# Performance work log

Hardware: AMD Instinct MI355X
Metric: run time of the kernel (lower is better)

Reference implementation:

```python
import jax, jax.numpy as jnp
import numpy as np

N, IN_DIM, HID, OUT, E = 20000, 1024, 512, 128, 160000


def _xavier(key, fan_out, fan_in):
    a = (6.0 / (fan_in + fan_out)) ** 0.5
    return jax.random.uniform(key, (fan_out, fan_in), jnp.float32, -a, a)


def setup_inputs() -> dict:
    key = jax.random.key(0)
    ks = jax.random.split(key, 8)
    features = jax.random.normal(ks[0], (N, IN_DIM), jnp.float32)
    edge_index = jax.random.randint(ks[1], (2, E), 0, N, jnp.int64)
    W1 = _xavier(ks[2], HID, IN_DIM)   # conv1.lin.weight [out,in]
    b1 = jnp.zeros((HID,), jnp.float32)
    W2 = _xavier(ks[3], OUT, HID)      # conv2.lin.weight
    b2 = jnp.zeros((OUT,), jnp.float32)
    b3 = jnp.zeros((HID,), jnp.float32)  # conv3 bias (weight tied = W2.T)
    b4 = jnp.zeros((IN_DIM,), jnp.float32)  # conv4 bias (weight tied = W1.T)
    head1 = _xavier(ks[4], OUT, OUT)
    return dict(features=features, edge_index=edge_index, W1=W1, b1=b1,
                W2=W2, b2=b2, b3=b3, b4=b4, head1=head1)


def _gcn_conv(x, W, b, src, dst, norm, n):
    # GCNConv: transform then symmetric-normalized neighbor aggregation
    h = x @ W.T                       # [N, out]
    msg = h[src] * norm[:, None]      # [E', out] gathered + scaled
    out = jax.ops.segment_sum(msg, dst, num_segments=n)
    return out + b


def reference(features, edge_index, W1, b1, W2, b2, b3, b4, head1):
    n = features.shape[0]
    loops = jnp.arange(n, dtype=edge_index.dtype)
    src = jnp.concatenate([edge_index[0], loops])  # add self-loops
    dst = jnp.concatenate([edge_index[1], loops])
    deg = jax.ops.segment_sum(jnp.ones_like(dst, dtype=features.dtype), dst,
                              num_segments=n)
    dinv = jnp.where(deg > 0, deg ** -0.5, 0.0)
    norm = dinv[src] * dinv[dst]

    h1 = _gcn_conv(features, W1, b1, src, dst, norm, n)
    h2 = _gcn_conv(h1, W2, b2, src, dst, norm, n)
    z = h2 @ head1
    # tied weights: conv3.W = W2^T, conv4.W = W1^T
    h3 = _gcn_conv(z, W2.T, b3, src, dst, norm, n)
    h4 = _gcn_conv(h3, W1.T, b4, src, dst, norm, n)
    return z, h2, h4
```

## Files before the change

kernel.cpp:

```cpp
#include <hip/hip_runtime.h>

typedef short   short8  __attribute__((ext_vector_type(8)));
typedef unsigned short ushort8 __attribute__((ext_vector_type(8)));
typedef float   floatx4 __attribute__((ext_vector_type(4)));

__device__ __forceinline__ float bf2f(unsigned short h) {
    unsigned int u = ((unsigned int)h) << 16;
    return __builtin_bit_cast(float, u);
}
__device__ __forceinline__ unsigned short f2bf(float f) {
    unsigned int u = __builtin_bit_cast(unsigned int, f);
    u += 0x7fffu + ((u >> 16) & 1u);
    return (unsigned short)(u >> 16);
}


__global__ __launch_bounds__(256) void k_detect_f32(const unsigned short* __restrict__ X,
                                                    int nPairs, int* __restrict__ flags) {
    int i = blockIdx.x * 256 + threadIdx.x;
    if (i < nPairs) {
        unsigned short w = X[2 * i];
        if ((w & 0x7F80u) == 0x7F80u) atomicOr(&flags[0], 1);
    }
}

__global__ __launch_bounds__(256) void k_detect_i32(const int* __restrict__ ei,
                                                    int E, int* __restrict__ flags) {
    int i = blockIdx.x * 256 + threadIdx.x;
    if (i < E) {
        if (ei[2 * i + 1] != 0) atomicOr(&flags[1], 1);
    }
}


__global__ __launch_bounds__(256) void k_cvt_f32(const void* __restrict__ in,
                                                 float* __restrict__ out, int n,
                                                 const int* __restrict__ flags) {
    int i = blockIdx.x * 256 + threadIdx.x;
    if (i < n)
        out[i] = flags[0] ? ((const float*)in)[i] : bf2f(((const unsigned short*)in)[i]);
}

__global__ __launch_bounds__(256) void k_tcvt(const void* __restrict__ in,
                                              unsigned short* __restrict__ out,
                                              int R, int C, const int* __restrict__ flags) {
    int idx = blockIdx.x * 256 + threadIdx.x;
    if (idx >= R * C) return;
    int r = idx / C, c = idx - r * C;
    unsigned short v = flags[0] ? f2bf(((const float*)in)[idx])
                                : ((const unsigned short*)in)[idx];
    out[(long)c * R + r] = v;
}


__global__ __launch_bounds__(256) void k_count(const int* __restrict__ ei, int E, int n,
                                               const int* __restrict__ flags,
                                               int* __restrict__ deg) {
    int e = blockIdx.x * 256 + threadIdx.x;
    if (e >= E) return;
    int sh = (flags[1] == 0) ? 1 : 0;
    int d = ei[(long)(E + e) << sh];
    if ((unsigned)d < (unsigned)n) atomicAdd(&deg[d], 1);
}

__global__ __launch_bounds__(256) void k_dinv(const int* __restrict__ deg,
                                              float* __restrict__ dinv, int n) {
    int i = blockIdx.x * 256 + threadIdx.x;
    if (i < n) dinv[i] = rsqrtf((float)(deg[i] + 1));
}

__global__ __launch_bounds__(1024) void k_scan(const int* __restrict__ deg,
                                               int* __restrict__ row_start,
                                               int* __restrict__ cursor, int n) {
    __shared__ int sums[1024];
    int t = threadIdx.x;
    int CH = (n + 1 + 1023) / 1024;
    int base = t * CH;
    int s = 0;
    for (int i = 0; i < CH; i++) {
        int idx = base + i;
        if (idx < n) s += deg[idx];
    }
    sums[t] = s;
    __syncthreads();
    for (int off = 1; off < 1024; off <<= 1) {
        int v = (t >= off) ? sums[t - off] : 0;
        __syncthreads();
        if (t >= off) sums[t] += v;
        __syncthreads();
    }
    int run = (t > 0) ? sums[t - 1] : 0;
    for (int i = 0; i < CH; i++) {
        int idx = base + i;
        if (idx < n) {
            row_start[idx] = run;
            cursor[idx] = run;
            run += deg[idx];
        } else if (idx == n) {
            row_start[n] = run;
        }
    }
}

__global__ __launch_bounds__(256) void k_fill(const int* __restrict__ ei, int E, int n,
                                              const int* __restrict__ flags,
                                              int* __restrict__ cursor,
                                              int* __restrict__ csr) {
    int e = blockIdx.x * 256 + threadIdx.x;
    if (e >= E) return;
    int sh = (flags[1] == 0) ? 1 : 0;
    int s = ei[(long)e << sh];
    int d = ei[(long)(E + e) << sh];
    if ((unsigned)d >= (unsigned)n || (unsigned)s >= (unsigned)n) return;
    int p = atomicAdd(&cursor[d], 1);
    csr[p] = s;
}


__device__ __forceinline__ ushort8 ld8(const void* p, long e, bool f32) {
    if (!f32) return *(const ushort8*)((const unsigned short*)p + e);
    const float* f = (const float*)p + e;
    ushort8 r;
#pragma unroll
    for (int i = 0; i < 8; i++) r[i] = f2bf(f[i]);
    return r;
}

__global__ __launch_bounds__(256) void gemm_nt(const void* __restrict__ A, int aMaybeF32,
                                               const void* __restrict__ Bt, int bMaybeF32,
                                               void* __restrict__ Cv, long coff,
                                               const float* __restrict__ bias,
                                               int M, int N, int K, int finalOut,
                                               const int* __restrict__ flags) {
    constexpr int BM = 128, BN = 64, BK = 32, LDT = 40;
    __shared__ unsigned short sA[BM * LDT];
    __shared__ unsigned short sB[BN * LDT];
    const bool af32 = aMaybeF32 && flags[0];
    const bool bf32 = bMaybeF32 && flags[0];
    const bool of32 = finalOut && flags[0];
    const bool hasb = bias != nullptr;
    const int t = threadIdx.x;
    const int m0 = blockIdx.y * BM;
    const int n0 = blockIdx.x * BN;
    const int w = t >> 6;
    const int lane = t & 63;
    const int id = lane & 15;
    const int q = lane >> 4;

    floatx4 acc[2][4];
    for (int s = 0; s < 2; s++)
        for (int j = 0; j < 4; j++) acc[s][j] = (floatx4)0.0f;

    const int ar = t >> 2;
    const int ac = (t & 3) * 8;

    for (int k0 = 0; k0 < K; k0 += BK) {
        long r0 = min(m0 + ar, M - 1);
        long r1 = min(m0 + ar + 64, M - 1);
        ushort8 va0 = ld8(A, r0 * K + k0 + ac, af32);
        ushort8 va1 = ld8(A, r1 * K + k0 + ac, af32);
        ushort8 vb  = ld8(Bt, (long)(n0 + ar) * K + k0 + ac, bf32);
        __syncthreads();
        *(ushort8*)(sA + ar * LDT + ac) = va0;
        *(ushort8*)(sA + (ar + 64) * LDT + ac) = va1;
        *(ushort8*)(sB + ar * LDT + ac) = vb;
        __syncthreads();

        short8 afrag[2], bfrag[4];
        for (int s = 0; s < 2; s++)
            afrag[s] = *(const short8*)(sA + (32 * w + 16 * s + id) * LDT + q * 8);
        for (int j = 0; j < 4; j++)
            bfrag[j] = *(const short8*)(sB + (16 * j + id) * LDT + q * 8);
        for (int s = 0; s < 2; s++)
            for (int j = 0; j < 4; j++)
                acc[s][j] = __builtin_amdgcn_mfma_f32_16x16x32_bf16(
                    afrag[s], bfrag[j], acc[s][j], 0, 0, 0);
    }

    for (int s = 0; s < 2; s++)
        for (int j = 0; j < 4; j++) {
            int col = n0 + 16 * j + id;
            float bv = hasb ? bias[col] : 0.0f;
            for (int r = 0; r < 4; r++) {
                int row = m0 + 32 * w + 16 * s + q * 4 + r;
                if (row < M) {
                    float v = acc[s][j][r] + bv;
                    if (of32) ((float*)Cv)[coff + (long)row * N + col] = v;
                    else ((unsigned short*)Cv)[coff + (long)row * N + col] = f2bf(v);
                }
            }
        }
}


template <int D>
__global__ __launch_bounds__(256) void k_agg(const unsigned short* __restrict__ T,
                                             const int* __restrict__ rs,
                                             const int* __restrict__ csr,
                                             const float* __restrict__ dinv,
                                             const float* __restrict__ bias,
                                             unsigned short* __restrict__ O, int n) {
    constexpr int TPN = D / 8;
    constexpr int NPB = 256 / TPN;
    int lt = threadIdx.x % TPN;
    int node = blockIdx.x * NPB + threadIdx.x / TPN;
    if (node >= n) return;
    int off = lt * 8;
    float acc[8];
#pragma unroll
    for (int i = 0; i < 8; i++) acc[i] = 0.0f;
    int beg = rs[node], end = rs[node + 1];
    for (int j = beg; j < end; j++) {
        int s = csr[j];
        if ((unsigned)s >= (unsigned)n) continue;
        float wgt = dinv[s];
        ushort8 v = *(const ushort8*)(T + (long)s * D + off);
#pragma unroll
        for (int i = 0; i < 8; i++) acc[i] += wgt * bf2f(v[i]);
    }
    float di = dinv[node];
    ushort8 sv = *(const ushort8*)(T + (long)node * D + off);
    ushort8 o;
#pragma unroll
    for (int i = 0; i < 8; i++) {
        float r = di * (acc[i] + di * bf2f(sv[i])) + (bias ? bias[off + i] : 0.0f);
        o[i] = f2bf(r);
    }
    *(ushort8*)(O + (long)node * D + off) = o;
}


__global__ __launch_bounds__(256) void k_out(const unsigned short* __restrict__ z,
                                             const unsigned short* __restrict__ h2,
                                             void* __restrict__ out, int nOut,
                                             const int* __restrict__ flags) {
    int i = blockIdx.x * 256 + threadIdx.x;
    if (i >= 2 * nOut) return;
    unsigned short v = (i < nOut) ? z[i] : h2[i - nOut];
    if (flags[0]) ((float*)out)[i] = bf2f(v);
    else ((unsigned short*)out)[i] = v;
}


extern "C" void kernel_launch(void* const* d_in, const int* in_sizes, int n_in,
                              void* d_out, int out_size, void* d_ws, size_t ws_size,
                              hipStream_t stream) {
    const int IN  = in_sizes[7];
    const int HID = in_sizes[3];
    const int OUT = in_sizes[5];
    const int Nn  = in_sizes[0] / IN;
    const int E   = in_sizes[1] / 2;

    const void* X   = d_in[0];
    const int*  ei  = (const int*)d_in[1];
    const void* W1  = d_in[2];
    const void* b1  = d_in[3];
    const void* W2  = d_in[4];
    const void* b2  = d_in[5];
    const void* b3  = d_in[6];
    const void* b4  = d_in[7];
    const void* Hd1 = d_in[8];

    char* base = (char*)d_ws;
    size_t o = 0;
    auto carve = [&](size_t bytes) -> char* {
        char* p = base + o;
        o = (o + bytes + 255) & ~(size_t)255;
        return p;
    };
    int*   flags  = (int*)carve(2 * 4);
    int*   deg    = (int*)carve((size_t)Nn * 4);
    int*   rowst  = (int*)carve((size_t)(Nn + 1) * 4);
    int*   cursor = (int*)carve((size_t)Nn * 4);
    float* dinv   = (float*)carve((size_t)Nn * 4);
    int*   csr    = (int*)carve((size_t)E * 4);
    float* biasf  = (float*)carve((size_t)(HID + OUT + HID + IN) * 4);
    float* bc1 = biasf, *bc2 = biasf + HID, *bc3 = biasf + HID + OUT,
         *bc4 = biasf + HID + OUT + HID;
    unsigned short* W1t  = (unsigned short*)carve((size_t)IN * HID * 2);
    unsigned short* W2t  = (unsigned short*)carve((size_t)HID * OUT * 2);
    unsigned short* H1t  = (unsigned short*)carve((size_t)OUT * OUT * 2);
    unsigned short* t1   = (unsigned short*)carve((size_t)Nn * HID * 2);
    unsigned short* h1   = (unsigned short*)carve((size_t)Nn * HID * 2);
    unsigned short* h3   = (unsigned short*)carve((size_t)Nn * HID * 2);
    unsigned short* t2   = (unsigned short*)carve((size_t)Nn * OUT * 2);
    unsigned short* h2ws = (unsigned short*)carve((size_t)Nn * OUT * 2);
    unsigned short* zws  = (unsigned short*)carve((size_t)Nn * OUT * 2);

    hipMemsetAsync(flags, 0, 8, stream);
    hipMemsetAsync(deg, 0, (size_t)Nn * 4, stream);
    int nPairs = 1 << 20;
    k_detect_f32<<<(nPairs + 255) / 256, 256, 0, stream>>>((const unsigned short*)X, nPairs, flags);
    k_detect_i32<<<(E + 255) / 256, 256, 0, stream>>>(ei, E, flags);

    k_cvt_f32<<<(HID + 255) / 256, 256, 0, stream>>>(b1, bc1, HID, flags);
    k_cvt_f32<<<(OUT + 255) / 256, 256, 0, stream>>>(b2, bc2, OUT, flags);
    k_cvt_f32<<<(HID + 255) / 256, 256, 0, stream>>>(b3, bc3, HID, flags);
    k_cvt_f32<<<(IN + 255) / 256, 256, 0, stream>>>(b4, bc4, IN, flags);

    k_tcvt<<<(HID * IN + 255) / 256, 256, 0, stream>>>(W1, W1t, HID, IN, flags);
    k_tcvt<<<(OUT * HID + 255) / 256, 256, 0, stream>>>(W2, W2t, OUT, HID, flags);
    k_tcvt<<<(OUT * OUT + 255) / 256, 256, 0, stream>>>(Hd1, H1t, OUT, OUT, flags);

    k_count<<<(E + 255) / 256, 256, 0, stream>>>(ei, E, Nn, flags, deg);
    k_dinv<<<(Nn + 255) / 256, 256, 0, stream>>>(deg, dinv, Nn);
    k_scan<<<1, 1024, 0, stream>>>(deg, rowst, cursor, Nn);
    k_fill<<<(E + 255) / 256, 256, 0, stream>>>(ei, E, Nn, flags, cursor, csr);

    dim3 blk(256);
    auto ggrid = [&](int Ncols) { return dim3((Ncols + 63) / 64, (Nn + 127) / 128); };
    const long zOff = 0, h2Off = (long)Nn * OUT, h4Off = (long)Nn * OUT * 2;

    gemm_nt<<<ggrid(HID), blk, 0, stream>>>(X, 1, W1, 1, t1, 0, nullptr, Nn, HID, IN, 0, flags);
    k_agg<512><<<(Nn * 64 + 255) / 256, blk, 0, stream>>>(t1, rowst, csr, dinv, bc1, h1, Nn);

    gemm_nt<<<ggrid(OUT), blk, 0, stream>>>(h1, 0, W2, 1, t2, 0, nullptr, Nn, OUT, HID, 0, flags);
    k_agg<128><<<(Nn * 16 + 255) / 256, blk, 0, stream>>>(t2, rowst, csr, dinv, bc2, h2ws, Nn);

    gemm_nt<<<ggrid(OUT), blk, 0, stream>>>(h2ws, 0, H1t, 0, zws, 0, nullptr, Nn, OUT, OUT, 0, flags);

    k_agg<128><<<(Nn * 16 + 255) / 256, blk, 0, stream>>>(zws, rowst, csr, dinv, nullptr, t2, Nn);
    gemm_nt<<<ggrid(HID), blk, 0, stream>>>(t2, 0, W2t, 0, h3, 0, bc3, Nn, HID, OUT, 0, flags);

    k_agg<512><<<(Nn * 64 + 255) / 256, blk, 0, stream>>>(h3, rowst, csr, dinv, nullptr, t1, Nn);
    gemm_nt<<<ggrid(IN), blk, 0, stream>>>(t1, 0, W1t, 0, d_out, h4Off, bc4, Nn, IN, HID, 1, flags);

    k_out<<<(2 * (int)h2Off + 255) / 256, blk, 0, stream>>>(zws, h2ws, d_out, (int)h2Off, flags);
}
```

Before: 611.0 us.

## Template GEMM on tile width and add XCD-aware block swizzle

Makes the GEMM N-tile width a template parameter and uses 128-wide tiles for the wide-output GEMMs (HID and IN columns), so each A tile loaded from memory feeds twice as many MFMAs. It also remaps workgroup IDs so consecutive tiles land on the same XCD, which should improve L2 reuse of the A rows. The cost is more accumulator registers per thread, which may lower occupancy, and fewer workgroups in the wide GEMMs.

```diff
diff --git a/kernel.cpp b/kernel.cpp
--- a/kernel.cpp
+++ b/kernel.cpp
@@ -126,13 +126,15 @@
     return r;
 }
 
+template <int BN>
 __global__ __launch_bounds__(256) void gemm_nt(const void* __restrict__ A, int aMaybeF32,
                                                const void* __restrict__ Bt, int bMaybeF32,
                                                void* __restrict__ Cv, long coff,
                                                const float* __restrict__ bias,
                                                int M, int N, int K, int finalOut,
                                                const int* __restrict__ flags) {
-    constexpr int BM = 128, BN = 64, BK = 32, LDT = 40;
+    constexpr int BM = 128, BK = 32, LDT = 40;
+    constexpr int JR = BN / 16;
     __shared__ unsigned short sA[BM * LDT];
     __shared__ unsigned short sB[BN * LDT];
     const bool af32 = aMaybeF32 && flags[0];
@@ -140,16 +142,24 @@
     const bool of32 = finalOut && flags[0];
     const bool hasb = bias != nullptr;
     const int t = threadIdx.x;
-    const int m0 = blockIdx.y * BM;
-    const int n0 = blockIdx.x * BN;
+
+    const int GX = gridDim.x;
+    const int nwg = GX * gridDim.y;
+    const int orig = blockIdx.y * GX + blockIdx.x;
+    const int q8 = nwg >> 3, r8 = nwg & 7;
+    const int xcd = orig & 7, cidx = orig >> 3;
+    const int swz = (xcd < r8 ? xcd * (q8 + 1) : r8 * (q8 + 1) + (xcd - r8) * q8) + cidx;
+    const int m0 = (swz / GX) * BM;
+    const int n0 = (swz % GX) * BN;
+
     const int w = t >> 6;
     const int lane = t & 63;
     const int id = lane & 15;
     const int q = lane >> 4;
 
-    floatx4 acc[2][4];
+    floatx4 acc[2][JR];
     for (int s = 0; s < 2; s++)
-        for (int j = 0; j < 4; j++) acc[s][j] = (floatx4)0.0f;
+        for (int j = 0; j < JR; j++) acc[s][j] = (floatx4)0.0f;
 
     const int ar = t >> 2;
     const int ac = (t & 3) * 8;
@@ -159,26 +169,31 @@
         long r1 = min(m0 + ar + 64, M - 1);
         ushort8 va0 = ld8(A, r0 * K + k0 + ac, af32);
         ushort8 va1 = ld8(A, r1 * K + k0 + ac, af32);
-        ushort8 vb  = ld8(Bt, (long)(n0 + ar) * K + k0 + ac, bf32);
+        ushort8 vb0, vb1;
+        vb0 = ld8(Bt, (long)min(n0 + ar, N - 1) * K + k0 + ac, bf32);
+        if (BN == 128)
+            vb1 = ld8(Bt, (long)min(n0 + ar + 64, N - 1) * K + k0 + ac, bf32);
         __syncthreads();
         *(ushort8*)(sA + ar * LDT + ac) = va0;
         *(ushort8*)(sA + (ar + 64) * LDT + ac) = va1;
-        *(ushort8*)(sB + ar * LDT + ac) = vb;
+        *(ushort8*)(sB + ar * LDT + ac) = vb0;
+        if (BN == 128)
+            *(ushort8*)(sB + (ar + 64) * LDT + ac) = vb1;
         __syncthreads();
 
-        short8 afrag[2], bfrag[4];
+        short8 afrag[2], bfrag[JR];
         for (int s = 0; s < 2; s++)
             afrag[s] = *(const short8*)(sA + (32 * w + 16 * s + id) * LDT + q * 8);
-        for (int j = 0; j < 4; j++)
+        for (int j = 0; j < JR; j++)
             bfrag[j] = *(const short8*)(sB + (16 * j + id) * LDT + q * 8);
         for (int s = 0; s < 2; s++)
-            for (int j = 0; j < 4; j++)
+            for (int j = 0; j < JR; j++)
                 acc[s][j] = __builtin_amdgcn_mfma_f32_16x16x32_bf16(
                     afrag[s], bfrag[j], acc[s][j], 0, 0, 0);
     }
 
     for (int s = 0; s < 2; s++)
-        for (int j = 0; j < 4; j++) {
+        for (int j = 0; j < JR; j++) {
             int col = n0 + 16 * j + id;
             float bv = hasb ? bias[col] : 0.0f;
             for (int r = 0; r < 4; r++) {
@@ -308,22 +323,22 @@
     k_fill<<<(E + 255) / 256, 256, 0, stream>>>(ei, E, Nn, flags, cursor, csr);
 
     dim3 blk(256);
-    auto ggrid = [&](int Ncols) { return dim3((Ncols + 63) / 64, (Nn + 127) / 128); };
+    auto ggrid = [&](int Ncols, int bn) { return dim3((Ncols + bn - 1) / bn, (Nn + 127) / 128); };
     const long zOff = 0, h2Off = (long)Nn * OUT, h4Off = (long)Nn * OUT * 2;
 
-    gemm_nt<<<ggrid(HID), blk, 0, stream>>>(X, 1, W1, 1, t1, 0, nullptr, Nn, HID, IN, 0, flags);
+    gemm_nt<128><<<ggrid(HID, 128), blk, 0, stream>>>(X, 1, W1, 1, t1, 0, nullptr, Nn, HID, IN, 0, flags);
     k_agg<512><<<(Nn * 64 + 255) / 256, blk, 0, stream>>>(t1, rowst, csr, dinv, bc1, h1, Nn);
 
-    gemm_nt<<<ggrid(OUT), blk, 0, stream>>>(h1, 0, W2, 1, t2, 0, nullptr, Nn, OUT, HID, 0, flags);
+    gemm_nt<64><<<ggrid(OUT, 64), blk, 0, stream>>>(h1, 0, W2, 1, t2, 0, nullptr, Nn, OUT, HID, 0, flags);
     k_agg<128><<<(Nn * 16 + 255) / 256, blk, 0, stream>>>(t2, rowst, csr, dinv, bc2, h2ws, Nn);
 
-    gemm_nt<<<ggrid(OUT), blk, 0, stream>>>(h2ws, 0, H1t, 0, zws, 0, nullptr, Nn, OUT, OUT, 0, flags);
+    gemm_nt<64><<<ggrid(OUT, 64), blk, 0, stream>>>(h2ws, 0, H1t, 0, zws, 0, nullptr, Nn, OUT, OUT, 0, flags);
 
     k_agg<128><<<(Nn * 16 + 255) / 256, blk, 0, stream>>>(zws, rowst, csr, dinv, nullptr, t2, Nn);
-    gemm_nt<<<ggrid(HID), blk, 0, stream>>>(t2, 0, W2t, 0, h3, 0, bc3, Nn, HID, OUT, 0, flags);
+    gemm_nt<128><<<ggrid(HID, 128), blk, 0, stream>>>(t2, 0, W2t, 0, h3, 0, bc3, Nn, HID, OUT, 0, flags);
 
     k_agg<512><<<(Nn * 64 + 255) / 256, blk, 0, stream>>>(h3, rowst, csr, dinv, nullptr, t1, Nn);
-    gemm_nt<<<ggrid(IN), blk, 0, stream>>>(t1, 0, W1t, 0, d_out, h4Off, bc4, Nn, IN, HID, 1, flags);
+    gemm_nt<128><<<ggrid(IN, 128), blk, 0, stream>>>(t1, 0, W1t, 0, d_out, h4Off, bc4, Nn, IN, HID, 1, flags);
 
     k_out<<<(2 * (int)h2Off + 255) / 256, blk, 0, stream>>>(zws, h2ws, d_out, (int)h2Off, flags);
 }
```

New measurement: 1.146 ms. 1.88x slower.
